# Optimization experiments

Measured on AMD Instinct MI355X. Metric: run time of the kernel, lower is better.

The kernel has to match this reference:

```python
import jax, jax.numpy as jnp
import numpy as np

N, L, S, C, H = 8, 1024, 1024, 512, 8
SCALE = float((C // H) ** 0.5)  # sqrt(64), as in source (based on embed_dim, not cat'd dim)


def _linear_params(key, c_in, c_out):
    kw, kb = jax.random.split(key)
    lim = 1.0 / np.sqrt(c_in)
    W = jax.random.uniform(kw, (c_out, c_in), jnp.float32, -lim, lim)
    b = jax.random.uniform(kb, (c_out,), jnp.float32, -lim, lim)
    return W, b


def setup_inputs() -> dict:
    key = jax.random.key(0)
    ks = jax.random.split(key, 12)
    inp = {
        'q_c': jax.random.normal(ks[0], (N, L, C), jnp.float32),
        'q_p': jax.random.normal(ks[1], (N, L, C), jnp.float32),
        'k_c': jax.random.normal(ks[2], (N, S, C), jnp.float32),
        'k_p': jax.random.normal(ks[3], (N, S, C), jnp.float32),
        'v': jax.random.normal(ks[4], (N, S, C), jnp.float32),
        'attn_mask': jax.random.normal(ks[5], (N, H, L, S), jnp.float32),
    }
    for i, name in enumerate(['qc', 'qp', 'kc', 'kp', 'v', 'o']):
        W, b = _linear_params(ks[6 + i], C, C)
        inp[f'W_{name}'] = W
        inp[f'b_{name}'] = b
    return inp


def _split_head(x, h):
    n, l, c = x.shape
    return x.reshape(n, l, h, c // h).transpose(0, 2, 1, 3)  # (N,H,L,c/h)


def reference(q_c, q_p, k_c, k_p, v, attn_mask,
              W_qc, b_qc, W_qp, b_qp, W_kc, b_kc, W_kp, b_kp, W_v, b_v, W_o, b_o):
    # dual projections + cat -> (N, L, 2C)
    q = jnp.concatenate([q_c @ W_qc.T + b_qc, q_p @ W_qp.T + b_qp], axis=-1)
    k = jnp.concatenate([k_c @ W_kc.T + b_kc, k_p @ W_kp.T + b_kp], axis=-1)
    vv = v @ W_v.T + b_v
    q = _split_head(q, H)   # (N,H,L,2C/H)
    k = _split_head(k, H)   # (N,H,S,2C/H)
    vv = _split_head(vv, H)  # (N,H,S,C/H)
    attn = jnp.einsum('nhld,nhsd->nhls', q / SCALE, k) + attn_mask
    attn = jax.nn.softmax(attn, axis=-1)
    out = jnp.einsum('nhls,nhsd->nhld', attn, vv)
    out = out.transpose(0, 2, 1, 3).reshape(N, L, C)
    return out @ W_o.T + b_o
```

## Files before the change

### kernel.cpp

```cpp
#include <hip/hip_runtime.h>
#include <hip/hip_bf16.h>

typedef __bf16 bf16;
typedef __bf16 bf16x8 __attribute__((ext_vector_type(8)));
typedef float  f32x4  __attribute__((ext_vector_type(4)));

#define LOG2E        1.4426950408889634f
#define QSCALE_LOG2E 0.18033688011112043f
#define DEFER_THR    20.0f

#define GLDS(g, l)                                                        \
  __builtin_amdgcn_global_load_lds(                                       \
      (const __attribute__((address_space(1))) void*)(g),                 \
      (__attribute__((address_space(3))) void*)(l), 16, 0, 0)

__device__ __forceinline__ void stage_f32_tile(const float* __restrict__ src, int ld,
                                               char* dst, int tid) {
  #pragma unroll
  for (int t = 0; t < 8; ++t) {
    int c8  = tid + t * 256;
    int row = c8 >> 4;
    int h8  = c8 & 15;
    const f32x4 v = *reinterpret_cast<const f32x4*>(src + row * ld + h8 * 4);
    union { bf16 h[4]; unsigned long long u; } pk;
    pk.h[0] = (bf16)v[0]; pk.h[1] = (bf16)v[1];
    pk.h[2] = (bf16)v[2]; pk.h[3] = (bf16)v[3];
    int byte = (row << 7) + ((((h8 >> 1) ^ (row & 7)) << 4) | ((h8 & 1) << 3));
    *reinterpret_cast<unsigned long long*>(dst + byte) = pk.u;
  }
}

__device__ __forceinline__ void stage_bf16_tile(const bf16* __restrict__ src, int ld,
                                                char* dst, int tid) {
  #pragma unroll
  for (int t = 0; t < 4; ++t) {
    int c   = tid + t * 256;
    int row = c >> 3;
    int ck  = c & 7;
    const bf16x8 v = *reinterpret_cast<const bf16x8*>(src + row * ld + ck * 8);
    int byte = (row << 7) + (((ck ^ (row & 7)) << 4));
    *reinterpret_cast<bf16x8*>(dst + byte) = v;
  }
}

__global__ __launch_bounds__(256) void proj_gemm(
    const float* __restrict__ qc, const float* __restrict__ qp,
    const float* __restrict__ kc, const float* __restrict__ kp,
    const float* __restrict__ vin,
    const float* __restrict__ Wqc, const float* __restrict__ bqc,
    const float* __restrict__ Wqp, const float* __restrict__ bqp,
    const float* __restrict__ Wkc, const float* __restrict__ bkc,
    const float* __restrict__ Wkp, const float* __restrict__ bkp,
    const float* __restrict__ Wv,  const float* __restrict__ bv,
    bf16* __restrict__ Qws, bf16* __restrict__ Kws, bf16* __restrict__ Vtws) {
  __shared__ __align__(16) bf16 lA[128 * 64];
  __shared__ __align__(16) bf16 lB[128 * 64];
  char* lAb = (char*)lA;
  char* lBb = (char*)lB;

  const int bx = blockIdx.x;
  const int g  = bx >> 8;
  const int mt = (bx & 255) >> 2;
  const int nt = bx & 3;

  const float *A, *W, *bias;
  if      (g == 0) { A = qc;  W = Wqc; bias = bqc; }
  else if (g == 1) { A = qp;  W = Wqp; bias = bqp; }
  else if (g == 2) { A = kc;  W = Wkc; bias = bkc; }
  else if (g == 3) { A = kp;  W = Wkp; bias = bkp; }
  else             { A = vin; W = Wv;  bias = bv;  }

  const int tid  = threadIdx.x;
  const int lane = tid & 63, wid = tid >> 6;
  const int wr = wid >> 1, wc = wid & 1;
  const int lrow = lane & 15, lgrp = lane >> 4;

  const float* Abase = A + (size_t)(mt * 128) * 512;
  const float* Wbase = W + (size_t)(nt * 128) * 512;

  const f32x4 fz = {0.f, 0.f, 0.f, 0.f};
  f32x4 acc[4][4];
  #pragma unroll
  for (int i = 0; i < 4; ++i)
    #pragma unroll
    for (int j = 0; j < 4; ++j) acc[i][j] = fz;

  for (int k0 = 0; k0 < 512; k0 += 64) {
    __syncthreads();
    stage_f32_tile(Abase + k0, 512, lAb, tid);
    stage_f32_tile(Wbase + k0, 512, lBb, tid);
    __syncthreads();
    #pragma unroll
    for (int kk = 0; kk < 2; ++kk) {
      bf16x8 af[4], bfr[4];
      #pragma unroll
      for (int mf = 0; mf < 4; ++mf) {
        int row  = wr * 64 + mf * 16 + lrow;
        int byte = (row << 7) + ((((kk << 2) | lgrp) ^ (row & 7)) << 4);
        af[mf] = *reinterpret_cast<const bf16x8*>(lAb + byte);
      }
      #pragma unroll
      for (int nf = 0; nf < 4; ++nf) {
        int row  = wc * 64 + nf * 16 + lrow;
        int byte = (row << 7) + ((((kk << 2) | lgrp) ^ (row & 7)) << 4);
        bfr[nf] = *reinterpret_cast<const bf16x8*>(lBb + byte);
      }
      #pragma unroll
      for (int mf = 0; mf < 4; ++mf)
        #pragma unroll
        for (int nf = 0; nf < 4; ++nf)
          acc[mf][nf] = __builtin_amdgcn_mfma_f32_16x16x32_bf16(
              af[mf], bfr[nf], acc[mf][nf], 0, 0, 0);
    }
  }

  float bcol[4];
  #pragma unroll
  for (int nf = 0; nf < 4; ++nf)
    bcol[nf] = bias[nt * 128 + wc * 64 + nf * 16 + lrow];

  #pragma unroll
  for (int mf = 0; mf < 4; ++mf) {
    #pragma unroll
    for (int nf = 0; nf < 4; ++nf) {
      #pragma unroll
      for (int r = 0; r < 4; ++r) {
        int grow = mt * 128 + wr * 64 + mf * 16 + lgrp * 4 + r;
        int col  = nt * 128 + wc * 64 + nf * 16 + lrow;
        float vv = acc[mf][nf][r] + bcol[nf];
        bf16 hb  = (bf16)vv;
        int n = grow >> 10, tt = grow & 1023;
        if (g < 2) {
          int j = (g << 9) + col;
          Qws[(size_t)((((n << 3) + (j >> 7)) << 10) | tt) * 128 + (j & 127)] = hb;
        } else if (g < 4) {
          int j = ((g - 2) << 9) + col;
          Kws[(size_t)((((n << 3) + (j >> 7)) << 10) | tt) * 128 + (j & 127)] = hb;
        } else {
          int h = col >> 6, d = col & 63;
          Vtws[(size_t)((((n << 3) + h) << 6) + d) * 1024 + tt] = hb;
        }
      }
    }
  }
}

__global__ __launch_bounds__(256) void attn_fwd(
    const bf16* __restrict__ Qws, const bf16* __restrict__ Kws,
    const bf16* __restrict__ Vtws, const float* __restrict__ mask,
    bf16* __restrict__ Ows) {
  __shared__ __align__(16) char Kl[2][8192];
  __shared__ __align__(16) char Vl[2][4096];
  __shared__ __align__(16) bf16 Pl[4][2][16][32];

  const int bx = blockIdx.x;
  const int nh = bx >> 4;
  const int qt = bx & 15;
  const int tid = threadIdx.x;
  const int lane = tid & 63, wid = tid >> 6;
  const int lrow = lane & 15, lgrp = lane >> 4;
  const int q0 = qt * 64 + wid * 16;

  const bf16* Qb = Qws + ((size_t)(nh * 1024 + q0 + lrow)) * 128 + lgrp * 8;
  bf16x8 qf[4];
  #pragma unroll
  for (int kk = 0; kk < 4; ++kk)
    qf[kk] = *reinterpret_cast<const bf16x8*>(Qb + kk * 32);

  const float* Mb = mask + ((size_t)(nh * 1024 + q0 + lgrp * 4)) * 1024 + lrow;

  const int kc0 = wid * 128 + lane;
  const int kr0 = kc0 >> 4, kd0 = kc0 & 15;
  const bf16* Kg0 = Kws + ((size_t)(nh * 1024 + kr0)) * 128 + (kd0 ^ (kr0 & 7)) * 8;
  const int kc1 = kc0 + 64;
  const int kr1 = kc1 >> 4, kd1 = kc1 & 15;
  const bf16* Kg1 = Kws + ((size_t)(nh * 1024 + kr1)) * 128 + (kd1 ^ (kr1 & 7)) * 8;
  const int vc  = wid * 64 + lane;
  const int vr  = vc >> 2, vs = vc & 3;
  const bf16* Vg = Vtws + ((size_t)(nh * 64 + vr)) * 1024 + vs * 8;

  char* Pb0 = (char*)&Pl[wid][0][0][0];

  const f32x4 fz = {0.f, 0.f, 0.f, 0.f};
  f32x4 oacc[4];
  #pragma unroll
  for (int dt = 0; dt < 4; ++dt) oacc[dt] = fz;
  float m2[4], lsum[4];
  #pragma unroll
  for (int r = 0; r < 4; ++r) { m2[r] = 0.f; lsum[r] = 0.f; }

  auto stageKV = [&](int buf, int s0) {
    GLDS(Kg0 + (size_t)s0 * 128, &Kl[buf][wid * 2048]);
    GLDS(Kg1 + (size_t)s0 * 128, &Kl[buf][wid * 2048 + 1024]);
    GLDS(Vg + s0,                &Vl[buf][wid * 1024]);
  };

  auto step = [&](int s0, int buf, float (&MK)[8], float (&MN)[8],
                  int sp, bool pref) {
    if (pref) stageKV(buf ^ 1, s0 + 32);
    if (sp >= 0) {
      #pragma unroll
      for (int r = 0; r < 4; ++r) {
        MN[r]     = Mb[(size_t)r * 1024 + sp];
        MN[4 + r] = Mb[(size_t)r * 1024 + sp + 16];
      }
    }

    const char* Kb = &Kl[buf][0];
    const char* Vb = &Vl[buf][0];
    bf16x8 kf0[4], kf1[4], vf[4];
    #pragma unroll
    for (int kk = 0; kk < 4; ++kk) {
      int ch = ((kk << 2) | lgrp) ^ (lrow & 7);
      kf0[kk] = *reinterpret_cast<const bf16x8*>(Kb + lrow * 256 + ch * 16);
      kf1[kk] = *reinterpret_cast<const bf16x8*>(Kb + (16 + lrow) * 256 + ch * 16);
    }
    #pragma unroll
    for (int dt = 0; dt < 4; ++dt)
      vf[dt] = *reinterpret_cast<const bf16x8*>(Vb + (dt * 16 + lrow) * 64 + lgrp * 16);

    f32x4 sc0 = fz, sc1 = fz;
    #pragma unroll
    for (int kk = 0; kk < 4; ++kk)
      sc0 = __builtin_amdgcn_mfma_f32_16x16x32_bf16(qf[kk], kf0[kk], sc0, 0, 0, 0);
    #pragma unroll
    for (int kk = 0; kk < 4; ++kk)
      sc1 = __builtin_amdgcn_mfma_f32_16x16x32_bf16(qf[kk], kf1[kk], sc1, 0, 0, 0);

    float a0r[4], a1r[4];
    bool ok = true;
    #pragma unroll
    for (int r = 0; r < 4; ++r) {
      a0r[r] = fmaf(sc0[r], QSCALE_LOG2E, MK[r] * LOG2E);
      a1r[r] = fmaf(sc1[r], QSCALE_LOG2E, MK[4 + r] * LOG2E);
      ok &= (fmaxf(a0r[r], a1r[r]) <= m2[r] + DEFER_THR);
    }
    if (__builtin_expect(!__all(ok), 0)) {
      #pragma unroll
      for (int r = 0; r < 4; ++r) {
        float tv = fmaxf(a0r[r], a1r[r]);
        tv = fmaxf(tv, __shfl_xor(tv, 1));
        tv = fmaxf(tv, __shfl_xor(tv, 2));
        tv = fmaxf(tv, __shfl_xor(tv, 4));
        tv = fmaxf(tv, __shfl_xor(tv, 8));
        float mn = fmaxf(m2[r], tv);
        float corr = exp2f(m2[r] - mn);
        m2[r] = mn;
        lsum[r] *= corr;
        #pragma unroll
        for (int dt = 0; dt < 4; ++dt) oacc[dt][r] *= corr;
      }
    }
    float p0[4], p1[4];
    #pragma unroll
    for (int r = 0; r < 4; ++r) {
      float e0 = exp2f(a0r[r] - m2[r]);
      float e1 = exp2f(a1r[r] - m2[r]);
      p0[r] = e0; p1[r] = e1;
      lsum[r] += e0 + e1;
    }

    char* Pb = Pb0 + ((s0 & 32) << 5);
    #pragma unroll
    for (int r = 0; r < 4; ++r) {
      int rowb = (lgrp * 4 + r) * 64;
      *reinterpret_cast<bf16*>(Pb + rowb + lrow * 2)      = (bf16)p0[r];
      *reinterpret_cast<bf16*>(Pb + rowb + 32 + lrow * 2) = (bf16)p1[r];
    }
    __builtin_amdgcn_wave_barrier();
    __builtin_amdgcn_sched_barrier(0);
    bf16x8 pf = *reinterpret_cast<const bf16x8*>(Pb + lrow * 64 + lgrp * 16);

    #pragma unroll
    for (int dt = 0; dt < 4; ++dt)
      oacc[dt] = __builtin_amdgcn_mfma_f32_16x16x32_bf16(pf, vf[dt], oacc[dt], 0, 0, 0);

    __syncthreads();
  };

  float mA[8], mB[8];
  stageKV(0, 0);
  #pragma unroll
  for (int r = 0; r < 4; ++r) {
    mA[r]     = Mb[(size_t)r * 1024];
    mA[4 + r] = Mb[(size_t)r * 1024 + 16];
  }
  __syncthreads();

  for (int tt = 0; tt < 16; ++tt) {
    int s0 = tt * 64;
    step(s0,      0, mA, mB, s0 + 32, true);
    step(s0 + 32, 1, mB, mA, (tt < 15) ? (s0 + 64) : -1, tt < 15);
  }

  #pragma unroll
  for (int r = 0; r < 4; ++r) {
    float ss = lsum[r];
    ss += __shfl_xor(ss, 1);
    ss += __shfl_xor(ss, 2);
    ss += __shfl_xor(ss, 4);
    ss += __shfl_xor(ss, 8);
    lsum[r] = 1.0f / ss;
  }

  const int n = nh >> 3, h = nh & 7;
  bf16* Ob = Ows + ((size_t)(n * 1024 + q0 + lgrp * 4)) * 512 + h * 64 + lrow;
  #pragma unroll
  for (int dt = 0; dt < 4; ++dt)
    #pragma unroll
    for (int r = 0; r < 4; ++r)
      Ob[(size_t)r * 512 + dt * 16] = (bf16)(oacc[dt][r] * lsum[r]);
}

__global__ __launch_bounds__(256) void out_gemm(
    const bf16* __restrict__ Ows, const float* __restrict__ Wo,
    const float* __restrict__ bo, float* __restrict__ out) {
  __shared__ __align__(16) bf16 lA[128 * 64];
  __shared__ __align__(16) bf16 lB[128 * 64];
  char* lAb = (char*)lA;
  char* lBb = (char*)lB;

  const int bx = blockIdx.x;
  const int mt = bx >> 2;
  const int nt = bx & 3;
  const int tid = threadIdx.x;
  const int lane = tid & 63, wid = tid >> 6;
  const int wr = wid >> 1, wc = wid & 1;
  const int lrow = lane & 15, lgrp = lane >> 4;

  const bf16*  Abase = Ows + (size_t)(mt * 128) * 512;
  const float* Wbase = Wo  + (size_t)(nt * 128) * 512;

  const f32x4 fz = {0.f, 0.f, 0.f, 0.f};
  f32x4 acc[4][4];
  #pragma unroll
  for (int i = 0; i < 4; ++i)
    #pragma unroll
    for (int j = 0; j < 4; ++j) acc[i][j] = fz;

  for (int k0 = 0; k0 < 512; k0 += 64) {
    __syncthreads();
    stage_bf16_tile(Abase + k0, 512, lAb, tid);
    stage_f32_tile(Wbase + k0, 512, lBb, tid);
    __syncthreads();
    #pragma unroll
    for (int kk = 0; kk < 2; ++kk) {
      bf16x8 af[4], bfr[4];
      #pragma unroll
      for (int mf = 0; mf < 4; ++mf) {
        int row  = wr * 64 + mf * 16 + lrow;
        int byte = (row << 7) + ((((kk << 2) | lgrp) ^ (row & 7)) << 4);
        af[mf] = *reinterpret_cast<const bf16x8*>(lAb + byte);
      }
      #pragma unroll
      for (int nf = 0; nf < 4; ++nf) {
        int row  = wc * 64 + nf * 16 + lrow;
        int byte = (row << 7) + ((((kk << 2) | lgrp) ^ (row & 7)) << 4);
        bfr[nf] = *reinterpret_cast<const bf16x8*>(lBb + byte);
      }
      #pragma unroll
      for (int mf = 0; mf < 4; ++mf)
        #pragma unroll
        for (int nf = 0; nf < 4; ++nf)
          acc[mf][nf] = __builtin_amdgcn_mfma_f32_16x16x32_bf16(
              af[mf], bfr[nf], acc[mf][nf], 0, 0, 0);
    }
  }

  float bcol[4];
  #pragma unroll
  for (int nf = 0; nf < 4; ++nf)
    bcol[nf] = bo[nt * 128 + wc * 64 + nf * 16 + lrow];

  #pragma unroll
  for (int mf = 0; mf < 4; ++mf) {
    #pragma unroll
    for (int nf = 0; nf < 4; ++nf) {
      #pragma unroll
      for (int r = 0; r < 4; ++r) {
        int grow = mt * 128 + wr * 64 + mf * 16 + lgrp * 4 + r;
        int col  = nt * 128 + wc * 64 + nf * 16 + lrow;
        out[(size_t)grow * 512 + col] = acc[mf][nf][r] + bcol[nf];
      }
    }
  }
}

extern "C" void kernel_launch(void* const* d_in, const int* in_sizes, int n_in,
                              void* d_out, int out_size, void* d_ws, size_t ws_size,
                              hipStream_t stream) {
  const float* qc   = (const float*)d_in[0];
  const float* qp   = (const float*)d_in[1];
  const float* kc   = (const float*)d_in[2];
  const float* kp   = (const float*)d_in[3];
  const float* vin  = (const float*)d_in[4];
  const float* mask = (const float*)d_in[5];
  const float* Wqc  = (const float*)d_in[6];
  const float* bqc  = (const float*)d_in[7];
  const float* Wqp  = (const float*)d_in[8];
  const float* bqp  = (const float*)d_in[9];
  const float* Wkc  = (const float*)d_in[10];
  const float* bkc  = (const float*)d_in[11];
  const float* Wkp  = (const float*)d_in[12];
  const float* bkp  = (const float*)d_in[13];
  const float* Wv   = (const float*)d_in[14];
  const float* bv   = (const float*)d_in[15];
  const float* Wo   = (const float*)d_in[16];
  const float* bo   = (const float*)d_in[17];

  bf16* Qws  = (bf16*)d_ws;
  bf16* Kws  = Qws  + (size_t)8 * 1024 * 1024;
  bf16* Vtws = Kws  + (size_t)8 * 1024 * 1024;
  bf16* Ows  = Vtws + (size_t)4 * 1024 * 1024;

  proj_gemm<<<dim3(1280), dim3(256), 0, stream>>>(
      qc, qp, kc, kp, vin, Wqc, bqc, Wqp, bqp, Wkc, bkc, Wkp, bkp, Wv, bv,
      Qws, Kws, Vtws);
  attn_fwd<<<dim3(1024), dim3(256), 0, stream>>>(Qws, Kws, Vtws, mask, Ows);
  out_gemm<<<dim3(256), dim3(256), 0, stream>>>(Ows, Wo, bo, (float*)d_out);
}
```

Baseline: 212.0 us.

## Triple-buffer K/V staging with vmcnt barriers and prefetch depth two in attention

Moves the attention kernel's K/V LDS staging from a double buffer to a rotating triple buffer with two tiles in flight. Full __syncthreads is replaced by explicit s_waitcnt vmcnt plus s_barrier, so memory latency can overlap compute over a longer window. It also changes the K and P LDS swizzles and reads the mask as float2 pairs with a reassigned column mapping. MFMA sections are wrapped in s_setprio raises. This adds LDS use and relies on hand-counted vmcnt values, which risks ordering bugs if the counts are wrong.

New measurement: 196.8 us. -7.1%, faster.

```diff
diff --git a/kernel.cpp b/kernel.cpp
--- a/kernel.cpp
+++ b/kernel.cpp
@@ -4,6 +4,7 @@
 typedef __bf16 bf16;
 typedef __bf16 bf16x8 __attribute__((ext_vector_type(8)));
 typedef float  f32x4  __attribute__((ext_vector_type(4)));
+typedef float  f32x2  __attribute__((ext_vector_type(2)));
 
 #define LOG2E        1.4426950408889634f
 #define QSCALE_LOG2E 0.18033688011112043f
@@ -13,6 +14,12 @@
   __builtin_amdgcn_global_load_lds(                                       \
       (const __attribute__((address_space(1))) void*)(g),                 \
       (__attribute__((address_space(3))) void*)(l), 16, 0, 0)
+
+#define VMCNT_BAR(n) do {                                                 \
+  asm volatile("s_waitcnt vmcnt(" #n ")" ::: "memory");                   \
+  __builtin_amdgcn_s_barrier();                                           \
+  __builtin_amdgcn_sched_barrier(0);                                      \
+} while (0)
 
 __device__ __forceinline__ void stage_f32_tile(const float* __restrict__ src, int ld,
                                                char* dst, int tid) {
@@ -149,9 +156,9 @@
     const bf16* __restrict__ Qws, const bf16* __restrict__ Kws,
     const bf16* __restrict__ Vtws, const float* __restrict__ mask,
     bf16* __restrict__ Ows) {
-  __shared__ __align__(16) char Kl[2][8192];
-  __shared__ __align__(16) char Vl[2][4096];
-  __shared__ __align__(16) bf16 Pl[4][2][16][32];
+  __shared__ __align__(16) char Kl[3][8192];
+  __shared__ __align__(16) char Vl[3][4096];
+  __shared__ __align__(16) char Pl[4][1024];
 
   const int bx = blockIdx.x;
   const int nh = bx >> 4;
@@ -167,19 +174,19 @@
   for (int kk = 0; kk < 4; ++kk)
     qf[kk] = *reinterpret_cast<const bf16x8*>(Qb + kk * 32);
 
-  const float* Mb = mask + ((size_t)(nh * 1024 + q0 + lgrp * 4)) * 1024 + lrow;
+  const float* Mb = mask + ((size_t)(nh * 1024 + q0 + lgrp * 4)) * 1024 + 2 * lrow;
 
   const int kc0 = wid * 128 + lane;
   const int kr0 = kc0 >> 4, kd0 = kc0 & 15;
-  const bf16* Kg0 = Kws + ((size_t)(nh * 1024 + kr0)) * 128 + (kd0 ^ (kr0 & 7)) * 8;
+  const bf16* Kg0 = Kws + ((size_t)(nh * 1024 + kr0)) * 128 + (kd0 ^ ((kr0 >> 1) & 7)) * 8;
   const int kc1 = kc0 + 64;
   const int kr1 = kc1 >> 4, kd1 = kc1 & 15;
-  const bf16* Kg1 = Kws + ((size_t)(nh * 1024 + kr1)) * 128 + (kd1 ^ (kr1 & 7)) * 8;
+  const bf16* Kg1 = Kws + ((size_t)(nh * 1024 + kr1)) * 128 + (kd1 ^ ((kr1 >> 1) & 7)) * 8;
   const int vc  = wid * 64 + lane;
   const int vr  = vc >> 2, vs = vc & 3;
   const bf16* Vg = Vtws + ((size_t)(nh * 64 + vr)) * 1024 + vs * 8;
 
-  char* Pb0 = (char*)&Pl[wid][0][0][0];
+  char* Pb = &Pl[wid][0];
 
   const f32x4 fz = {0.f, 0.f, 0.f, 0.f};
   f32x4 oacc[4];
@@ -189,50 +196,41 @@
   #pragma unroll
   for (int r = 0; r < 4; ++r) { m2[r] = 0.f; lsum[r] = 0.f; }
 
-  auto stageKV = [&](int buf, int s0) {
-    GLDS(Kg0 + (size_t)s0 * 128, &Kl[buf][wid * 2048]);
-    GLDS(Kg1 + (size_t)s0 * 128, &Kl[buf][wid * 2048 + 1024]);
-    GLDS(Vg + s0,                &Vl[buf][wid * 1024]);
+  auto stageKV = [&](char* Ksg, char* Vsg, int sN) {
+    GLDS(Kg0 + (size_t)sN * 128, Ksg + wid * 2048);
+    GLDS(Kg1 + (size_t)sN * 128, Ksg + wid * 2048 + 1024);
+    GLDS(Vg + sN,                Vsg + wid * 1024);
   };
 
-  auto step = [&](int s0, int buf, float (&MK)[8], float (&MN)[8],
-                  int sp, bool pref) {
-    if (pref) stageKV(buf ^ 1, s0 + 32);
-    if (sp >= 0) {
-      #pragma unroll
-      for (int r = 0; r < 4; ++r) {
-        MN[r]     = Mb[(size_t)r * 1024 + sp];
-        MN[4 + r] = Mb[(size_t)r * 1024 + sp + 16];
-      }
-    }
-
-    const char* Kb = &Kl[buf][0];
-    const char* Vb = &Vl[buf][0];
+  auto compute = [&](const char* Kb, const char* Vb, f32x2 (&MK)[4]) {
     bf16x8 kf0[4], kf1[4], vf[4];
     #pragma unroll
     for (int kk = 0; kk < 4; ++kk) {
-      int ch = ((kk << 2) | lgrp) ^ (lrow & 7);
-      kf0[kk] = *reinterpret_cast<const bf16x8*>(Kb + lrow * 256 + ch * 16);
-      kf1[kk] = *reinterpret_cast<const bf16x8*>(Kb + (16 + lrow) * 256 + ch * 16);
+      int cb = ((((kk << 2) | lgrp) ^ (lrow & 7)) << 4);
+      kf0[kk] = *reinterpret_cast<const bf16x8*>(Kb + lrow * 512 + cb);
+      kf1[kk] = *reinterpret_cast<const bf16x8*>(Kb + lrow * 512 + 256 + cb);
     }
     #pragma unroll
     for (int dt = 0; dt < 4; ++dt)
       vf[dt] = *reinterpret_cast<const bf16x8*>(Vb + (dt * 16 + lrow) * 64 + lgrp * 16);
 
     f32x4 sc0 = fz, sc1 = fz;
+    __builtin_amdgcn_s_setprio(1);
     #pragma unroll
     for (int kk = 0; kk < 4; ++kk)
       sc0 = __builtin_amdgcn_mfma_f32_16x16x32_bf16(qf[kk], kf0[kk], sc0, 0, 0, 0);
     #pragma unroll
     for (int kk = 0; kk < 4; ++kk)
       sc1 = __builtin_amdgcn_mfma_f32_16x16x32_bf16(qf[kk], kf1[kk], sc1, 0, 0, 0);
+    __builtin_amdgcn_s_setprio(0);
 
     float a0r[4], a1r[4];
     bool ok = true;
     #pragma unroll
     for (int r = 0; r < 4; ++r) {
-      a0r[r] = fmaf(sc0[r], QSCALE_LOG2E, MK[r] * LOG2E);
-      a1r[r] = fmaf(sc1[r], QSCALE_LOG2E, MK[4 + r] * LOG2E);
+      f32x2 mv = MK[r];
+      a0r[r] = fmaf(sc0[r], QSCALE_LOG2E, mv.x * LOG2E);
+      a1r[r] = fmaf(sc1[r], QSCALE_LOG2E, mv.y * LOG2E);
       ok &= (fmaxf(a0r[r], a1r[r]) <= m2[r] + DEFER_THR);
     }
     if (__builtin_expect(!__all(ok), 0)) {
@@ -251,47 +249,69 @@
         for (int dt = 0; dt < 4; ++dt) oacc[dt][r] *= corr;
       }
     }
-    float p0[4], p1[4];
     #pragma unroll
     for (int r = 0; r < 4; ++r) {
       float e0 = exp2f(a0r[r] - m2[r]);
       float e1 = exp2f(a1r[r] - m2[r]);
-      p0[r] = e0; p1[r] = e1;
       lsum[r] += e0 + e1;
-    }
-
-    char* Pb = Pb0 + ((s0 & 32) << 5);
-    #pragma unroll
-    for (int r = 0; r < 4; ++r) {
-      int rowb = (lgrp * 4 + r) * 64;
-      *reinterpret_cast<bf16*>(Pb + rowb + lrow * 2)      = (bf16)p0[r];
-      *reinterpret_cast<bf16*>(Pb + rowb + 32 + lrow * 2) = (bf16)p1[r];
+      union { bf16 h[2]; unsigned u; } pk;
+      pk.h[0] = (bf16)e0; pk.h[1] = (bf16)e1;
+      int row = lgrp * 4 + r;
+      int byte = row * 64 + ((((lrow >> 2) ^ (row & 3)) << 4) | ((lrow & 3) << 2));
+      *reinterpret_cast<unsigned*>(Pb + byte) = pk.u;
     }
     __builtin_amdgcn_wave_barrier();
     __builtin_amdgcn_sched_barrier(0);
-    bf16x8 pf = *reinterpret_cast<const bf16x8*>(Pb + lrow * 64 + lgrp * 16);
-
+    bf16x8 pf = *reinterpret_cast<const bf16x8*>(
+        Pb + lrow * 64 + ((lgrp ^ (lrow & 3)) << 4));
+
+    __builtin_amdgcn_s_setprio(1);
     #pragma unroll
     for (int dt = 0; dt < 4; ++dt)
       oacc[dt] = __builtin_amdgcn_mfma_f32_16x16x32_bf16(pf, vf[dt], oacc[dt], 0, 0, 0);
-
-    __syncthreads();
+    __builtin_amdgcn_s_setprio(0);
   };
 
-  float mA[8], mB[8];
-  stageKV(0, 0);
+  auto step_main = [&](const char* Kb, const char* Vb, char* Ksg, char* Vsg,
+                       int sN, f32x2 (&MK)[4]) {
+    stageKV(Ksg, Vsg, sN);
+    f32x2 mnew[4];
+    #pragma unroll
+    for (int r = 0; r < 4; ++r)
+      mnew[r] = *reinterpret_cast<const f32x2*>(Mb + (size_t)r * 1024 + sN);
+    compute(Kb, Vb, MK);
+    #pragma unroll
+    for (int r = 0; r < 4; ++r) MK[r] = mnew[r];
+  };
+
+  char *k0 = &Kl[0][0], *k1 = &Kl[1][0], *k2 = &Kl[2][0];
+  char *v0 = &Vl[0][0], *v1 = &Vl[1][0], *v2 = &Vl[2][0];
+  char *kc_ = k0, *kn_ = k1, *kf_ = k2;
+  char *vc_ = v0, *vn_ = v1, *vf_ = v2;
+
+  stageKV(kc_, vc_, 0);
+  stageKV(kn_, vn_, 32);
+  f32x2 mX[4], mY[4];
   #pragma unroll
   for (int r = 0; r < 4; ++r) {
-    mA[r]     = Mb[(size_t)r * 1024];
-    mA[4 + r] = Mb[(size_t)r * 1024 + 16];
-  }
-  __syncthreads();
-
-  for (int tt = 0; tt < 16; ++tt) {
+    mX[r] = *reinterpret_cast<const f32x2*>(Mb + (size_t)r * 1024);
+    mY[r] = *reinterpret_cast<const f32x2*>(Mb + (size_t)r * 1024 + 32);
+  }
+  VMCNT_BAR(8);
+
+  for (int tt = 0; tt < 15; ++tt) {
     int s0 = tt * 64;
-    step(s0,      0, mA, mB, s0 + 32, true);
-    step(s0 + 32, 1, mB, mA, (tt < 15) ? (s0 + 64) : -1, tt < 15);
-  }
+    step_main(kc_, vc_, kf_, vf_, s0 + 64, mX);
+    VMCNT_BAR(11);
+    step_main(kn_, vn_, kc_, vc_, s0 + 96, mY);
+    VMCNT_BAR(11);
+    char* t1 = kc_; kc_ = kf_; kf_ = kn_; kn_ = t1;
+    char* t2 = vc_; vc_ = vf_; vf_ = vn_; vn_ = t2;
+  }
+
+  compute(kc_, vc_, mX);
+  VMCNT_BAR(4);
+  compute(kn_, vn_, mY);
 
   #pragma unroll
   for (int r = 0; r < 4; ++r) {
```
